# Optimization experiments

Measured on AMD Instinct MI355X. Metric: run time of the kernel, lower is better.

The kernel has to match this reference:

```python
import jax, jax.numpy as jnp
import numpy as np

SIGMA1 = 0.02   # sigma1 init arg
K = 128         # number of discretization bins
TMIN = 1e-10
LEAKY_SLOPE = 0.01  # torch nn.LeakyReLU default


def setup_inputs() -> dict:
    key = jax.random.key(0)
    k1, k2, k3, k4, k5 = jax.random.split(key, 5)
    B, D, H = 256, 1024, 2048
    x = jax.random.uniform(k1, (B, D), jnp.float32, -1.0, 1.0)
    t = jax.random.uniform(k2, (B, 1), jnp.float32)          # Uniform(0,1) time sample
    noise = jax.random.normal(k3, (B, D), jnp.float32)       # for Normal sample of mu
    W1 = jax.random.normal(k4, (D + 1, H), jnp.float32) * (1.0 / np.sqrt(D + 1))
    b1 = jnp.zeros((H,), jnp.float32)
    W2 = jax.random.normal(k5, (H, 2 * D), jnp.float32) * (1.0 / np.sqrt(H))
    b2 = jnp.zeros((2 * D,), jnp.float32)
    return dict(x=x, t=t, noise=noise, W1=W1, b1=b1, W2=W2, b2=b2)


def _discretised_output_distribution(mu, t, gamma, W1, b1, W2, b2):
    B, D = mu.shape
    # NN: Linear -> LeakyReLU -> Linear, split into mu_eps / ln_sigma_eps
    h = jnp.concatenate([mu, t], axis=1) @ W1 + b1
    h = jnp.where(h >= 0, h, LEAKY_SLOPE * h)
    out = h @ W2 + b2
    mu_eps, ln_sig_eps = out[:, :D], out[:, D:]

    r = jnp.sqrt((1.0 - gamma) / gamma)                      # (B,1)
    mu_x = mu / gamma - r * mu_eps                           # (B,D)
    sigma_x = r * jnp.exp(ln_sig_eps)                        # (B,D)

    low_t = t < TMIN                                         # (B,1) rows with tiny t
    mu_x = jnp.where(low_t, 0.0, mu_x)
    sigma_x = jnp.where(low_t, 1.0, sigma_x)

    k = jnp.arange(K, dtype=jnp.float32)
    kl = 2.0 * (k - 1.0) / K - 1.0                           # left bin edge
    kr = 2.0 * k / K - 1.0                                   # right bin edge
    kc = (2.0 * k - 1.0) / K - 1.0                           # bin center weight

    inv = 1.0 / (sigma_x * jnp.sqrt(jnp.float32(2.0)))       # (B,D)

    def cdf(bound):  # bound: (K,) scalars -> clamped discretized CDF (B,D,K)
        F = 0.5 * (1.0 + jax.lax.erf((bound[None, None, :] - mu_x[:, :, None]) * inv[:, :, None]))
        return jnp.where(bound <= -1.0, 0.0, jnp.where(bound >= 1.0, 1.0, F))

    p = kc * (cdf(kr) - cdf(kl))                             # (B,D,K)
    return jnp.sum(p, axis=-1)                               # (B,D) expected value


def reference(x, t, noise, W1, b1, W2, b2):
    gamma = 1.0 - SIGMA1 ** (2.0 * t)                        # (B,1)
    # mu ~ Normal(gamma*x, std=gamma*(1-gamma)), reparameterized with noise
    mu = gamma * x + gamma * (1.0 - gamma) * noise
    pO = _discretised_output_distribution(mu, t, gamma, W1, b1, W2, b2)
    se = (x - pO) ** 2                                       # elementwise MSE
    loss = -jnp.log(jnp.float32(SIGMA1)) * jnp.mean(SIGMA1 ** (-2.0 * t) * se)
    return loss
```

## Files before the change

kernel.cpp:

```cpp
#include <hip/hip_runtime.h>
#include <hip/hip_bf16.h>
#include <math.h>


typedef __bf16 bf16_t;
typedef __bf16 bf16x8 __attribute__((ext_vector_type(8)));
typedef __bf16 bf16x4 __attribute__((ext_vector_type(4)));
typedef float  f32x4  __attribute__((ext_vector_type(4)));

#define LDK 40
#define L2S -5.6438561897747248f

__device__ __forceinline__ float erf_f(float x) {
  float ax = __builtin_fabsf(x);
  float t = __builtin_amdgcn_rcpf(fmaf(0.3275911f, ax, 1.0f));
  float p = fmaf(fmaf(fmaf(fmaf(1.061405429f, t, -1.453152027f), t, 1.421413741f),
                      t, -0.284496736f), t, 0.254829592f);
  p *= t;
  float e = __expf(-ax * ax);
  float r = fmaf(-p, e, 1.0f);
  return __builtin_copysignf(r, x);
}

__global__ __launch_bounds__(256, 2)
void prep_k(const float* __restrict__ x, const float* __restrict__ noise,
            const float* __restrict__ t, bf16_t* __restrict__ A1) {
  int b = blockIdx.x;
  float tv = t[b];
  float p = exp2f(2.0f * tv * L2S);
  float g = 1.0f - p, gom = g * p;
  int e = (b * 256 + threadIdx.x) * 4;
  float4 xv = *(const float4*)(x + e);
  float4 nv = *(const float4*)(noise + e);
  bf16x4 o;
  o[0] = (__bf16)fmaf(gom, nv.x, g * xv.x);
  o[1] = (__bf16)fmaf(gom, nv.y, g * xv.y);
  o[2] = (__bf16)fmaf(gom, nv.z, g * xv.z);
  o[3] = (__bf16)fmaf(gom, nv.w, g * xv.w);
  *(bf16x4*)(A1 + e) = o;
}

__global__ __launch_bounds__(256, 2)
void gemm_k(const bf16_t* __restrict__ A, int lda,
            const float* __restrict__ W, int N,
            float* __restrict__ P, int Ktiles, int Kchunk) {
  __shared__ bf16_t As[256 * LDK];
  __shared__ bf16_t Bs[32 * LDK];
  int tid = threadIdx.x;
  int lane = tid & 63, wave = tid >> 6;
  int n0 = blockIdx.x * 32;
  int k0 = blockIdx.z * Kchunk;
  int bn = tid & 31, bkg = tid >> 5;
  int fm = lane & 15, kq = lane >> 4;

  f32x4 acc[4][2];
#pragma unroll
  for (int i = 0; i < 4; ++i)
#pragma unroll
    for (int j = 0; j < 2; ++j) acc[i][j] = (f32x4)0.0f;

  for (int kt = 0; kt < Ktiles; ++kt) {
    int kb = k0 + kt * 32;
    const bf16_t* Ar = A + (size_t)tid * lda + kb;
#pragma unroll
    for (int j = 0; j < 4; ++j)
      *(bf16x8*)(&As[tid * LDK + j * 8]) = *(const bf16x8*)(Ar + j * 8);
    {
      const float* Wp = W + (size_t)(kb + bkg * 4) * N + n0 + bn;
      bf16x4 bv;
#pragma unroll
      for (int i = 0; i < 4; ++i) bv[i] = (__bf16)Wp[(size_t)i * N];
      *(bf16x4*)(&Bs[bn * LDK + bkg * 4]) = bv;
    }
    __syncthreads();
    bf16x8 aF[4], bF[2];
#pragma unroll
    for (int i = 0; i < 4; ++i)
      aF[i] = *(const bf16x8*)(&As[(wave * 64 + i * 16 + fm) * LDK + kq * 8]);
#pragma unroll
    for (int j = 0; j < 2; ++j)
      bF[j] = *(const bf16x8*)(&Bs[(j * 16 + fm) * LDK + kq * 8]);
#pragma unroll
    for (int i = 0; i < 4; ++i)
#pragma unroll
      for (int j = 0; j < 2; ++j)
        acc[i][j] = __builtin_amdgcn_mfma_f32_16x16x32_bf16(aF[i], bF[j], acc[i][j], 0, 0, 0);
    __syncthreads();
  }
  float* Pp = P + (size_t)blockIdx.z * 256 * N + n0;
#pragma unroll
  for (int i = 0; i < 4; ++i) {
    int mrow = wave * 64 + i * 16 + kq * 4;
#pragma unroll
    for (int j = 0; j < 2; ++j)
#pragma unroll
      for (int r = 0; r < 4; ++r)
        Pp[(size_t)(mrow + r) * N + j * 16 + fm] = acc[i][j][r];
  }
}

__global__ __launch_bounds__(256, 2)
void reduce1_k(const float* __restrict__ P1, const float* __restrict__ W1,
               const float* __restrict__ b1, const float* __restrict__ t,
               bf16_t* __restrict__ h, float* __restrict__ out) {
  if (blockIdx.x == 0 && threadIdx.x == 0) *out = 0.0f;
  int e = (blockIdx.x * 256 + threadIdx.x) * 4;
  int b = e >> 11, n = e & 2047;
  float4 s = *(const float4*)(P1 + e);
#pragma unroll
  for (int sp = 1; sp < 8; ++sp) {
    float4 v = *(const float4*)(P1 + (size_t)sp * 524288 + e);
    s.x += v.x; s.y += v.y; s.z += v.z; s.w += v.w;
  }
  float tv = t[b];
  float4 wl = *(const float4*)(W1 + 1024 * 2048 + n);
  float4 bb = *(const float4*)(b1 + n);
  s.x += tv * wl.x + bb.x;
  s.y += tv * wl.y + bb.y;
  s.z += tv * wl.z + bb.z;
  s.w += tv * wl.w + bb.w;
  bf16x4 o;
  o[0] = (__bf16)(s.x >= 0.f ? s.x : 0.01f * s.x);
  o[1] = (__bf16)(s.y >= 0.f ? s.y : 0.01f * s.y);
  o[2] = (__bf16)(s.z >= 0.f ? s.z : 0.01f * s.z);
  o[3] = (__bf16)(s.w >= 0.f ? s.w : 0.01f * s.w);
  *(bf16x4*)(h + e) = o;
}

__global__ __launch_bounds__(256, 4)
void loss_k(const float* __restrict__ x, const float* __restrict__ noise,
            const float* __restrict__ P2, const float* __restrict__ b2,
            const float* __restrict__ t, float* __restrict__ out) {
  int gid = blockIdx.x * 256 + threadIdx.x;
  int b = gid >> 10, d = gid & 1023;
  float tv = t[b];
  float om = exp2f(2.0f * tv * L2S);
  float gamma = 1.0f - om;
  float r = sqrtf(om / gamma);
  float w = 1.0f / om;
  bool lowt = tv < 1e-10f;
  int base2 = b * 2048 + d;
  float me = b2[d], lg = b2[1024 + d];
#pragma unroll
  for (int sp = 0; sp < 8; ++sp) {
    me += P2[(size_t)sp * 524288 + base2];
    lg += P2[(size_t)sp * 524288 + base2 + 1024];
  }
  float xs = x[gid], ns = noise[gid];

  float mu_x = xs + om * ns - r * me;
  float sig = r * __expf(lg);
  if (lowt) { mu_x = 0.f; sig = 1.f; }
  float invs = 0.70710678118654752f / sig;
  float a = invs * 0.015625f;
  float c0 = (1.f + mu_x) * invs;
  float m64 = 64.f * (1.f + mu_x);
  float wdt = 316.78383797157331f * sig;
  float lo = m64 - wdt, hi = m64 + wdt;
  int klo = (lo < 1.f) ? 1 : ((lo > 126.f) ? 127 : (int)ceilf(lo));
  int khi = (hi < 1.f) ? 0 : ((hi > 126.f) ? 126 : (int)floorf(hi));
  float ss = (float)(126 - khi) - (float)(klo - 1);
  if (khi >= klo) {
    if (a <= 1.0f) {
      float za = fmaf(a, (float)klo - 0.5f, -c0);
      float zb = fmaf(a, (float)khi + 0.5f, -c0);
      const float ISP = 0.56418958354775628f;
      float ea = __expf(-za * za), eb = __expf(-zb * zb);
      float Ga = fmaf(za, erf_f(za), ISP * ea);
      float Gb = fmaf(zb, erf_f(zb), ISP * eb);
      float S = (Gb - Ga) * __builtin_amdgcn_rcpf(a)
              - a * 0.047015889f * (eb - ea);
      ss += S;
    } else {
      for (int k = klo; k <= khi; ++k) ss += erf_f(fmaf(a, (float)k, -c0));
    }
  }
  float z127 = fmaf(a, 127.f, -c0);
  float pO = fmaf(0.48828125f, 1.f + erf_f(z127),
                  fmaf(-0.0078125f, ss, -0.984375f));
  float df = xs - pO;
  float accv = w * df * df;
#pragma unroll
  for (int off = 32; off > 0; off >>= 1) accv += __shfl_down(accv, off, 64);
  __shared__ float red[4];
  if ((threadIdx.x & 63) == 0) red[threadIdx.x >> 6] = accv;
  __syncthreads();
  if (threadIdx.x == 0) {
    const float SCALE = 3.9120230054281461f / 262144.0f;
    atomicAdd(out, (red[0] + red[1] + red[2] + red[3]) * SCALE);
  }
}

extern "C" void kernel_launch(void* const* d_in, const int* in_sizes, int n_in,
                              void* d_out, int out_size, void* d_ws, size_t ws_size,
                              hipStream_t stream) {
  const float* x     = (const float*)d_in[0];
  const float* t     = (const float*)d_in[1];
  const float* noise = (const float*)d_in[2];
  const float* W1    = (const float*)d_in[3];
  const float* b1    = (const float*)d_in[4];
  const float* W2    = (const float*)d_in[5];
  const float* b2    = (const float*)d_in[6];
  float* out = (float*)d_out;

  char* ws = (char*)d_ws;
  bf16_t* A1 = (bf16_t*)ws;
  bf16_t* h  = (bf16_t*)(ws + 524288);
  float*  P1 = (float*)(ws + 524288 + 1048576);
  float*  P2 = (float*)(ws + 524288 + 1048576 + 16777216);

  prep_k<<<256, 256, 0, stream>>>(x, noise, t, A1);
  gemm_k<<<dim3(64, 1, 8), 256, 0, stream>>>(A1, 1024, W1, 2048, P1, 4, 128);
  reduce1_k<<<512, 256, 0, stream>>>(P1, W1, b1, t, h, out);
  gemm_k<<<dim3(64, 1, 8), 256, 0, stream>>>(h, 2048, W2, 2048, P2, 8, 256);
  loss_k<<<1024, 256, 0, stream>>>(x, noise, P2, b2, t, out);
}
```

Baseline: 124.2 us.

## Fuse all five stages into one cooperative kernel with grid syncs

Replaces the five separate launches (prep, two split-K GEMMs, the reduction and the loss) with a single cooperative persistent kernel of 256 blocks. Grid-wide syncs separate the stages, and each block loops over two GEMM tiles and several loss rows. This removes per-launch overhead and the gaps between kernels. In exchange it caps parallelism at 256 blocks, about one per CU, and adds grid-sync costs that may serialize the GEMM work more than before.

```diff
diff --git a/kernel.cpp b/kernel.cpp
--- a/kernel.cpp
+++ b/kernel.cpp
@@ -1,7 +1,10 @@
 #include <hip/hip_runtime.h>
 #include <hip/hip_bf16.h>
+#include <hip/hip_cooperative_groups.h>
 #include <math.h>
 
+
+namespace cg = cooperative_groups;
 
 typedef __bf16 bf16_t;
 typedef __bf16 bf16x8 __attribute__((ext_vector_type(8)));
@@ -22,34 +25,13 @@
   return __builtin_copysignf(r, x);
 }
 
-__global__ __launch_bounds__(256, 2)
-void prep_k(const float* __restrict__ x, const float* __restrict__ noise,
-            const float* __restrict__ t, bf16_t* __restrict__ A1) {
-  int b = blockIdx.x;
-  float tv = t[b];
-  float p = exp2f(2.0f * tv * L2S);
-  float g = 1.0f - p, gom = g * p;
-  int e = (b * 256 + threadIdx.x) * 4;
-  float4 xv = *(const float4*)(x + e);
-  float4 nv = *(const float4*)(noise + e);
-  bf16x4 o;
-  o[0] = (__bf16)fmaf(gom, nv.x, g * xv.x);
-  o[1] = (__bf16)fmaf(gom, nv.y, g * xv.y);
-  o[2] = (__bf16)fmaf(gom, nv.z, g * xv.z);
-  o[3] = (__bf16)fmaf(gom, nv.w, g * xv.w);
-  *(bf16x4*)(A1 + e) = o;
-}
-
-__global__ __launch_bounds__(256, 2)
-void gemm_k(const bf16_t* __restrict__ A, int lda,
-            const float* __restrict__ W, int N,
-            float* __restrict__ P, int Ktiles, int Kchunk) {
-  __shared__ bf16_t As[256 * LDK];
-  __shared__ bf16_t Bs[32 * LDK];
+__device__ __forceinline__ void gemm_phase(const bf16_t* __restrict__ A, int lda,
+                                           const float* __restrict__ W, int N,
+                                           float* __restrict__ P, int Ktiles,
+                                           int k0, int n0,
+                                           bf16_t* As, bf16_t* Bs) {
   int tid = threadIdx.x;
   int lane = tid & 63, wave = tid >> 6;
-  int n0 = blockIdx.x * 32;
-  int k0 = blockIdx.z * Kchunk;
   int bn = tid & 31, bkg = tid >> 5;
   int fm = lane & 15, kq = lane >> 4;
 
@@ -87,7 +69,7 @@
         acc[i][j] = __builtin_amdgcn_mfma_f32_16x16x32_bf16(aF[i], bF[j], acc[i][j], 0, 0, 0);
     __syncthreads();
   }
-  float* Pp = P + (size_t)blockIdx.z * 256 * N + n0;
+  float* Pp = P + n0;
 #pragma unroll
   for (int i = 0; i < 4; ++i) {
     int mrow = wave * 64 + i * 16 + kq * 4;
@@ -99,95 +81,147 @@
   }
 }
 
-__global__ __launch_bounds__(256, 2)
-void reduce1_k(const float* __restrict__ P1, const float* __restrict__ W1,
-               const float* __restrict__ b1, const float* __restrict__ t,
-               bf16_t* __restrict__ h, float* __restrict__ out) {
-  if (blockIdx.x == 0 && threadIdx.x == 0) *out = 0.0f;
-  int e = (blockIdx.x * 256 + threadIdx.x) * 4;
-  int b = e >> 11, n = e & 2047;
-  float4 s = *(const float4*)(P1 + e);
-#pragma unroll
-  for (int sp = 1; sp < 8; ++sp) {
-    float4 v = *(const float4*)(P1 + (size_t)sp * 524288 + e);
-    s.x += v.x; s.y += v.y; s.z += v.z; s.w += v.w;
-  }
-  float tv = t[b];
-  float4 wl = *(const float4*)(W1 + 1024 * 2048 + n);
-  float4 bb = *(const float4*)(b1 + n);
-  s.x += tv * wl.x + bb.x;
-  s.y += tv * wl.y + bb.y;
-  s.z += tv * wl.z + bb.z;
-  s.w += tv * wl.w + bb.w;
-  bf16x4 o;
-  o[0] = (__bf16)(s.x >= 0.f ? s.x : 0.01f * s.x);
-  o[1] = (__bf16)(s.y >= 0.f ? s.y : 0.01f * s.y);
-  o[2] = (__bf16)(s.z >= 0.f ? s.z : 0.01f * s.z);
-  o[3] = (__bf16)(s.w >= 0.f ? s.w : 0.01f * s.w);
-  *(bf16x4*)(h + e) = o;
-}
-
-__global__ __launch_bounds__(256, 4)
-void loss_k(const float* __restrict__ x, const float* __restrict__ noise,
-            const float* __restrict__ P2, const float* __restrict__ b2,
-            const float* __restrict__ t, float* __restrict__ out) {
-  int gid = blockIdx.x * 256 + threadIdx.x;
-  int b = gid >> 10, d = gid & 1023;
-  float tv = t[b];
-  float om = exp2f(2.0f * tv * L2S);
-  float gamma = 1.0f - om;
-  float r = sqrtf(om / gamma);
-  float w = 1.0f / om;
-  bool lowt = tv < 1e-10f;
-  int base2 = b * 2048 + d;
-  float me = b2[d], lg = b2[1024 + d];
-#pragma unroll
-  for (int sp = 0; sp < 8; ++sp) {
-    me += P2[(size_t)sp * 524288 + base2];
-    lg += P2[(size_t)sp * 524288 + base2 + 1024];
-  }
-  float xs = x[gid], ns = noise[gid];
-
-  float mu_x = xs + om * ns - r * me;
-  float sig = r * __expf(lg);
-  if (lowt) { mu_x = 0.f; sig = 1.f; }
-  float invs = 0.70710678118654752f / sig;
-  float a = invs * 0.015625f;
-  float c0 = (1.f + mu_x) * invs;
-  float m64 = 64.f * (1.f + mu_x);
-  float wdt = 316.78383797157331f * sig;
-  float lo = m64 - wdt, hi = m64 + wdt;
-  int klo = (lo < 1.f) ? 1 : ((lo > 126.f) ? 127 : (int)ceilf(lo));
-  int khi = (hi < 1.f) ? 0 : ((hi > 126.f) ? 126 : (int)floorf(hi));
-  float ss = (float)(126 - khi) - (float)(klo - 1);
-  if (khi >= klo) {
-    if (a <= 1.0f) {
-      float za = fmaf(a, (float)klo - 0.5f, -c0);
-      float zb = fmaf(a, (float)khi + 0.5f, -c0);
-      const float ISP = 0.56418958354775628f;
-      float ea = __expf(-za * za), eb = __expf(-zb * zb);
-      float Ga = fmaf(za, erf_f(za), ISP * ea);
-      float Gb = fmaf(zb, erf_f(zb), ISP * eb);
-      float S = (Gb - Ga) * __builtin_amdgcn_rcpf(a)
-              - a * 0.047015889f * (eb - ea);
-      ss += S;
-    } else {
-      for (int k = klo; k <= khi; ++k) ss += erf_f(fmaf(a, (float)k, -c0));
-    }
-  }
-  float z127 = fmaf(a, 127.f, -c0);
-  float pO = fmaf(0.48828125f, 1.f + erf_f(z127),
-                  fmaf(-0.0078125f, ss, -0.984375f));
-  float df = xs - pO;
-  float accv = w * df * df;
-#pragma unroll
-  for (int off = 32; off > 0; off >>= 1) accv += __shfl_down(accv, off, 64);
-  __shared__ float red[4];
-  if ((threadIdx.x & 63) == 0) red[threadIdx.x >> 6] = accv;
-  __syncthreads();
-  if (threadIdx.x == 0) {
-    const float SCALE = 3.9120230054281461f / 262144.0f;
-    atomicAdd(out, (red[0] + red[1] + red[2] + red[3]) * SCALE);
+__global__ __launch_bounds__(256)
+void mega_k(const float* __restrict__ x, const float* __restrict__ t,
+            const float* __restrict__ noise,
+            const float* __restrict__ W1, const float* __restrict__ b1,
+            const float* __restrict__ W2, const float* __restrict__ b2,
+            float* __restrict__ out,
+            bf16_t* __restrict__ A1, bf16_t* __restrict__ h,
+            float* __restrict__ P1, float* __restrict__ P2) {
+  cg::grid_group grid = cg::this_grid();
+  __shared__ __align__(16) bf16_t smem[256 * LDK + 32 * LDK];
+  bf16_t* As = smem;
+  bf16_t* Bs = smem + 256 * LDK;
+  int blk = blockIdx.x;
+  int tid = threadIdx.x;
+
+  {
+    float tv = t[blk];
+    float p = exp2f(2.0f * tv * L2S);
+    float g = 1.0f - p, gom = g * p;
+    int e = (blk * 256 + tid) * 4;
+    float4 xv = *(const float4*)(x + e);
+    float4 nv = *(const float4*)(noise + e);
+    bf16x4 o;
+    o[0] = (__bf16)fmaf(gom, nv.x, g * xv.x);
+    o[1] = (__bf16)fmaf(gom, nv.y, g * xv.y);
+    o[2] = (__bf16)fmaf(gom, nv.z, g * xv.z);
+    o[3] = (__bf16)fmaf(gom, nv.w, g * xv.w);
+    *(bf16x4*)(A1 + e) = o;
+  }
+  __threadfence();
+  grid.sync();
+
+#pragma unroll
+  for (int it = 0; it < 2; ++it) {
+    int task = blk + it * 256;
+    int nt = task & 63, z = task >> 6;
+    gemm_phase(A1, 1024, W1, 2048, P1 + (size_t)z * 524288, 4, z * 128, nt * 32, As, Bs);
+  }
+  __threadfence();
+  grid.sync();
+
+  if (blk == 0 && tid == 0) *out = 0.0f;
+#pragma unroll
+  for (int it = 0; it < 2; ++it) {
+    int e = (blk * 512 + it * 256 + tid) * 4;
+    int b = e >> 11, n = e & 2047;
+    float4 s = *(const float4*)(P1 + e);
+#pragma unroll
+    for (int sp = 1; sp < 8; ++sp) {
+      float4 v = *(const float4*)(P1 + (size_t)sp * 524288 + e);
+      s.x += v.x; s.y += v.y; s.z += v.z; s.w += v.w;
+    }
+    float tv = t[b];
+    float4 wl = *(const float4*)(W1 + 1024 * 2048 + n);
+    float4 bb = *(const float4*)(b1 + n);
+    s.x += tv * wl.x + bb.x;
+    s.y += tv * wl.y + bb.y;
+    s.z += tv * wl.z + bb.z;
+    s.w += tv * wl.w + bb.w;
+    bf16x4 o;
+    o[0] = (__bf16)(s.x >= 0.f ? s.x : 0.01f * s.x);
+    o[1] = (__bf16)(s.y >= 0.f ? s.y : 0.01f * s.y);
+    o[2] = (__bf16)(s.z >= 0.f ? s.z : 0.01f * s.z);
+    o[3] = (__bf16)(s.w >= 0.f ? s.w : 0.01f * s.w);
+    *(bf16x4*)(h + e) = o;
+  }
+  __threadfence();
+  grid.sync();
+
+#pragma unroll
+  for (int it = 0; it < 2; ++it) {
+    int task = blk + it * 256;
+    int nt = task & 63, z = task >> 6;
+    gemm_phase(h, 2048, W2, 2048, P2 + (size_t)z * 524288, 8, z * 256, nt * 32, As, Bs);
+  }
+  __threadfence();
+  grid.sync();
+
+  {
+    float tv = t[blk];
+    float om = exp2f(2.0f * tv * L2S);
+    float gamma = 1.0f - om;
+    float r = sqrtf(om / gamma);
+    float w = 1.0f / om;
+    bool lowt = tv < 1e-10f;
+    float accv = 0.f;
+#pragma unroll
+    for (int it = 0; it < 4; ++it) {
+      int gid = blk * 1024 + it * 256 + tid;
+      int d = it * 256 + tid;
+      int base2 = blk * 2048 + d;
+      float me = b2[d], lg = b2[1024 + d];
+#pragma unroll
+      for (int sp = 0; sp < 8; ++sp) {
+        me += P2[(size_t)sp * 524288 + base2];
+        lg += P2[(size_t)sp * 524288 + base2 + 1024];
+      }
+      float xs = x[gid], ns = noise[gid];
+      float mu_x = xs + om * ns - r * me;
+      float sig = r * __expf(lg);
+      if (lowt) { mu_x = 0.f; sig = 1.f; }
+      float invs = 0.70710678118654752f / sig;
+      float a = invs * 0.015625f;
+      float c0 = (1.f + mu_x) * invs;
+      float m64 = 64.f * (1.f + mu_x);
+      float wdt = 316.78383797157331f * sig;
+      float lo = m64 - wdt, hi = m64 + wdt;
+      int klo = (lo < 1.f) ? 1 : ((lo > 126.f) ? 127 : (int)ceilf(lo));
+      int khi = (hi < 1.f) ? 0 : ((hi > 126.f) ? 126 : (int)floorf(hi));
+      float ss = (float)(126 - khi) - (float)(klo - 1);
+      if (khi >= klo) {
+        if (a <= 1.0f) {
+          float za = fmaf(a, (float)klo - 0.5f, -c0);
+          float zb = fmaf(a, (float)khi + 0.5f, -c0);
+          const float ISP = 0.56418958354775628f;
+          float ea = __expf(-za * za), eb = __expf(-zb * zb);
+          float Ga = fmaf(za, erf_f(za), ISP * ea);
+          float Gb = fmaf(zb, erf_f(zb), ISP * eb);
+          float S = (Gb - Ga) * __builtin_amdgcn_rcpf(a)
+                  - a * 0.047015889f * (eb - ea);
+          ss += S;
+        } else {
+          for (int k = klo; k <= khi; ++k) ss += erf_f(fmaf(a, (float)k, -c0));
+        }
+      }
+      float z127 = fmaf(a, 127.f, -c0);
+      float pO = fmaf(0.48828125f, 1.f + erf_f(z127),
+                      fmaf(-0.0078125f, ss, -0.984375f));
+      float df = xs - pO;
+      accv = fmaf(w * df, df, accv);
+    }
+#pragma unroll
+    for (int off = 32; off > 0; off >>= 1) accv += __shfl_down(accv, off, 64);
+    float* red = (float*)smem;
+    __syncthreads();
+    if ((tid & 63) == 0) red[tid >> 6] = accv;
+    __syncthreads();
+    if (tid == 0) {
+      const float SCALE = 3.9120230054281461f / 262144.0f;
+      atomicAdd(out, (red[0] + red[1] + red[2] + red[3]) * SCALE);
+    }
   }
 }
 
@@ -209,9 +243,10 @@
   float*  P1 = (float*)(ws + 524288 + 1048576);
   float*  P2 = (float*)(ws + 524288 + 1048576 + 16777216);
 
-  prep_k<<<256, 256, 0, stream>>>(x, noise, t, A1);
-  gemm_k<<<dim3(64, 1, 8), 256, 0, stream>>>(A1, 1024, W1, 2048, P1, 4, 128);
-  reduce1_k<<<512, 256, 0, stream>>>(P1, W1, b1, t, h, out);
-  gemm_k<<<dim3(64, 1, 8), 256, 0, stream>>>(h, 2048, W2, 2048, P2, 8, 256);
-  loss_k<<<1024, 256, 0, stream>>>(x, noise, P2, b2, t, out);
-}
+  void* args[] = {
+    (void*)&x, (void*)&t, (void*)&noise, (void*)&W1, (void*)&b1,
+    (void*)&W2, (void*)&b2, (void*)&out,
+    (void*)&A1, (void*)&h, (void*)&P1, (void*)&P2
+  };
+  hipLaunchCooperativeKernel((void*)mega_k, dim3(256), dim3(256), args, 0, stream);
+}
```

New measurement: 345.4 us. +178.0%, slower.

## Replace split-K partial buffers with atomic accumulation into zeroed outputs

Applied to the files above, without the earlier changes.

The GEMM kernels now accumulate their split-K partial sums directly into one output buffer using hardware float atomics, instead of writing eight separate partial slices. prep_k zeroes these buffers, and the reduce and loss kernels read a single value instead of summing eight. This removes large partial-sum write and read traffic, at the cost of atomic contention and a non-deterministic summation order. C2 is zeroed over a larger range than it needs.

```diff
diff --git a/kernel.cpp b/kernel.cpp
--- a/kernel.cpp
+++ b/kernel.cpp
@@ -24,12 +24,20 @@
 
 __global__ __launch_bounds__(256, 2)
 void prep_k(const float* __restrict__ x, const float* __restrict__ noise,
-            const float* __restrict__ t, bf16_t* __restrict__ A1) {
+            const float* __restrict__ t, bf16_t* __restrict__ A1,
+            float4* __restrict__ C1z, float4* __restrict__ C2z) {
   int b = blockIdx.x;
+  int gid = b * 256 + threadIdx.x;
+  f32x4 z = (f32x4)0.0f;
+#pragma unroll
+  for (int i = 0; i < 2; ++i) *(f32x4*)&C1z[gid + i * 65536] = z;
+#pragma unroll
+  for (int i = 0; i < 4; ++i) *(f32x4*)&C2z[gid + i * 65536] = z;
+
   float tv = t[b];
   float p = exp2f(2.0f * tv * L2S);
   float g = 1.0f - p, gom = g * p;
-  int e = (b * 256 + threadIdx.x) * 4;
+  int e = gid * 4;
   float4 xv = *(const float4*)(x + e);
   float4 nv = *(const float4*)(noise + e);
   bf16x4 o;
@@ -43,7 +51,7 @@
 __global__ __launch_bounds__(256, 2)
 void gemm_k(const bf16_t* __restrict__ A, int lda,
             const float* __restrict__ W, int N,
-            float* __restrict__ P, int Ktiles, int Kchunk) {
+            float* __restrict__ C, int Ktiles, int Kchunk) {
   __shared__ bf16_t As[256 * LDK];
   __shared__ bf16_t Bs[32 * LDK];
   int tid = threadIdx.x;
@@ -87,7 +95,7 @@
         acc[i][j] = __builtin_amdgcn_mfma_f32_16x16x32_bf16(aF[i], bF[j], acc[i][j], 0, 0, 0);
     __syncthreads();
   }
-  float* Pp = P + (size_t)blockIdx.z * 256 * N + n0;
+  float* Cp = C + n0;
 #pragma unroll
   for (int i = 0; i < 4; ++i) {
     int mrow = wave * 64 + i * 16 + kq * 4;
@@ -95,23 +103,18 @@
     for (int j = 0; j < 2; ++j)
 #pragma unroll
       for (int r = 0; r < 4; ++r)
-        Pp[(size_t)(mrow + r) * N + j * 16 + fm] = acc[i][j][r];
+        unsafeAtomicAdd(&Cp[(size_t)(mrow + r) * N + j * 16 + fm], acc[i][j][r]);
   }
 }
 
 __global__ __launch_bounds__(256, 2)
-void reduce1_k(const float* __restrict__ P1, const float* __restrict__ W1,
+void reduce1_k(const float* __restrict__ C1, const float* __restrict__ W1,
                const float* __restrict__ b1, const float* __restrict__ t,
                bf16_t* __restrict__ h, float* __restrict__ out) {
   if (blockIdx.x == 0 && threadIdx.x == 0) *out = 0.0f;
   int e = (blockIdx.x * 256 + threadIdx.x) * 4;
   int b = e >> 11, n = e & 2047;
-  float4 s = *(const float4*)(P1 + e);
-#pragma unroll
-  for (int sp = 1; sp < 8; ++sp) {
-    float4 v = *(const float4*)(P1 + (size_t)sp * 524288 + e);
-    s.x += v.x; s.y += v.y; s.z += v.z; s.w += v.w;
-  }
+  float4 s = *(const float4*)(C1 + e);
   float tv = t[b];
   float4 wl = *(const float4*)(W1 + 1024 * 2048 + n);
   float4 bb = *(const float4*)(b1 + n);
@@ -129,7 +132,7 @@
 
 __global__ __launch_bounds__(256, 4)
 void loss_k(const float* __restrict__ x, const float* __restrict__ noise,
-            const float* __restrict__ P2, const float* __restrict__ b2,
+            const float* __restrict__ C2, const float* __restrict__ b2,
             const float* __restrict__ t, float* __restrict__ out) {
   int gid = blockIdx.x * 256 + threadIdx.x;
   int b = gid >> 10, d = gid & 1023;
@@ -140,12 +143,8 @@
   float w = 1.0f / om;
   bool lowt = tv < 1e-10f;
   int base2 = b * 2048 + d;
-  float me = b2[d], lg = b2[1024 + d];
-#pragma unroll
-  for (int sp = 0; sp < 8; ++sp) {
-    me += P2[(size_t)sp * 524288 + base2];
-    lg += P2[(size_t)sp * 524288 + base2 + 1024];
-  }
+  float me = C2[base2] + b2[d];
+  float lg = C2[base2 + 1024] + b2[1024 + d];
   float xs = x[gid], ns = noise[gid];
 
   float mu_x = xs + om * ns - r * me;
@@ -206,12 +205,12 @@
   char* ws = (char*)d_ws;
   bf16_t* A1 = (bf16_t*)ws;
   bf16_t* h  = (bf16_t*)(ws + 524288);
-  float*  P1 = (float*)(ws + 524288 + 1048576);
-  float*  P2 = (float*)(ws + 524288 + 1048576 + 16777216);
-
-  prep_k<<<256, 256, 0, stream>>>(x, noise, t, A1);
-  gemm_k<<<dim3(64, 1, 8), 256, 0, stream>>>(A1, 1024, W1, 2048, P1, 4, 128);
-  reduce1_k<<<512, 256, 0, stream>>>(P1, W1, b1, t, h, out);
-  gemm_k<<<dim3(64, 1, 8), 256, 0, stream>>>(h, 2048, W2, 2048, P2, 8, 256);
-  loss_k<<<1024, 256, 0, stream>>>(x, noise, P2, b2, t, out);
-}
+  float*  C1 = (float*)(ws + 524288 + 1048576);
+  float*  C2 = (float*)(ws + 524288 + 1048576 + 2097152);
+
+  prep_k<<<256, 256, 0, stream>>>(x, noise, t, A1, (float4*)C1, (float4*)C2);
+  gemm_k<<<dim3(64, 1, 8), 256, 0, stream>>>(A1, 1024, W1, 2048, C1, 4, 128);
+  reduce1_k<<<512, 256, 0, stream>>>(C1, W1, b1, t, h, out);
+  gemm_k<<<dim3(64, 1, 8), 256, 0, stream>>>(h, 2048, W2, 2048, C2, 8, 256);
+  loss_k<<<1024, 256, 0, stream>>>(x, noise, C2, b2, t, out);
+}
```

After: 139.5 us. 1.12x slower.
